# Kernel tuning notes

Hardware: AMD Instinct MI355X
Metric: run time of the kernel (lower is better)

The kernel has to match this reference:

```python
import jax, jax.numpy as jnp
import numpy as np

N = 100000          # nodes
E = 1600000         # edges per adjacency (avg degree 16)
DIMS = [256, 128, 64]
ALPHA = 0.8
WD = 1e-4


def setup_inputs() -> dict:
    key = jax.random.key(0)
    ks = jax.random.split(key, 11)
    X = jax.random.normal(ks[0], (N, DIMS[0]), jnp.float32)
    rows = jax.random.randint(ks[1], (E,), 0, N, jnp.int32)
    cols = jax.random.randint(ks[2], (E,), 0, N, jnp.int32)
    prune_rows = jax.random.randint(ks[3], (E,), 0, N, jnp.int32)
    prune_cols = jax.random.randint(ks[4], (E,), 0, N, jnp.int32)
    # learned params (torch.randn init, scaled 0.1 for fp32 numeric headroom)
    W0 = jax.random.normal(ks[5], (DIMS[0], DIMS[1]), jnp.float32) * 0.1
    W1 = jax.random.normal(ks[6], (DIMS[1], DIMS[2]), jnp.float32) * 0.1
    v00 = jax.random.normal(ks[7], (DIMS[1], 1), jnp.float32) * 0.1
    v01 = jax.random.normal(ks[8], (DIMS[1], 1), jnp.float32) * 0.1
    pv00 = jax.random.normal(ks[9], (DIMS[1], 1), jnp.float32) * 0.1
    pv01 = jax.random.normal(ks[10], (DIMS[1], 1), jnp.float32) * 0.1
    return {"X": X, "W0": W0, "W1": W1, "v00": v00, "v01": v01,
            "pv00": pv00, "pv01": pv01, "rows": rows, "cols": cols,
            "prune_rows": prune_rows, "prune_cols": prune_cols}


def _edge_softmax(rows, logits, n):
    # row-wise softmax over sparse edge logits
    m = jax.ops.segment_max(logits, rows, num_segments=n)
    e = jnp.exp(logits - m[rows])
    s = jax.ops.segment_sum(e, rows, num_segments=n)
    return e / s[rows]


def _attention(rows, cols, H, va, vb, n):
    # logit_e = (H @ va)[src_e] + (H @ vb)[dst_e]  (binary adjacency values)
    f1 = (H @ va)[:, 0]
    f2 = (H @ vb)[:, 0]
    return _edge_softmax(rows, f1[rows] + f2[cols], n)


def _spmm(rows, cols, vals, H, n):
    # out[i] = sum_{e: rows[e]==i} vals[e] * H[cols[e]]
    return jax.ops.segment_sum(vals[:, None] * H[cols], rows, num_segments=n)


def reference(X, W0, W1, v00, v01, pv00, pv01, rows, cols, prune_rows, prune_cols):
    n = X.shape[0]
    # ---- encoder ----
    H1 = X @ W0                                   # layer 0 projection
    c = _attention(rows, cols, H1, v00, v01, n)   # C[0]
    pc = _attention(prune_rows, prune_cols, H1, pv00, pv01, n)  # prune_C[0]
    H1a = (1.0 - ALPHA) * _spmm(rows, cols, c, H1, n) \
        + ALPHA * _spmm(prune_rows, prune_cols, pc, H1, n)
    H1a = jax.nn.elu(H1a)                         # nonlinear, layer 0 != last
    H_enc = H1a @ W1                              # layer 1 == last: no attention
    # ---- decoder ----
    D = H_enc @ W1.T                              # layer 1
    D = (1.0 - ALPHA) * _spmm(rows, cols, c, D, n) \
        + ALPHA * _spmm(prune_rows, prune_cols, pc, D, n)
    D = jax.nn.elu(D)                             # nonlinear, layer 1 != 0
    X_ = D @ W0.T                                 # layer 0: plain matmul
    # ---- loss ----
    loss = jnp.sqrt(jnp.sum((X - X_) ** 2)) \
         + WD * (jnp.sum(W0 ** 2) + jnp.sum(W1 ** 2))
    return (loss, H_enc, X_)
```

## Files before the change

### kernel.cpp

```cpp
#include <hip/hip_runtime.h>
#include <math.h>

#define N_NODES 100000
#define N_EDGES 1600000
#define TOT (2 * N_NODES)
#define SCAN_NB 256
#define SCAN_CH 4
#define RPB 25000

static inline int cdiv(long a, long b) { return (int)((a + b - 1) / b); }

typedef unsigned int uint;
typedef unsigned short ushort;
typedef __attribute__((ext_vector_type(8))) short short8v;
typedef __attribute__((ext_vector_type(4))) float f32x4;

__device__ inline float bf2f(uint u) { return __uint_as_float(u << 16); }
__device__ inline ushort f2bf(float f) {
    uint u = __float_as_uint(f);
    uint r = ((u >> 16) & 1u) + 0x7fffu;
    return (ushort)((u + r) >> 16);
}

template <int K, int M, bool AF32, int OUT, bool ELU, bool LOSS>
__global__ __launch_bounds__(256) void gemm_mfma(const void* __restrict__ Av,
                                                 const ushort* __restrict__ Bcm,
                                                 void* __restrict__ Cv,
                                                 void* __restrict__ Cv2,
                                                 const float* __restrict__ Xref,
                                                 float* __restrict__ partial,
                                                 int nrows) {
    constexpr int BM = 128;
    constexpr int KP = K + 8;
    constexpr int NCT = M / 16;
    __shared__ ushort Blds[M * KP];
    __shared__ ushort Alds[BM * 32];
    const int w = threadIdx.x >> 6;
    const int l = threadIdx.x & 63;
    const int rowg = l & 15;
    const int kg = l >> 4;
    const int rbase = blockIdx.x * BM;
    {
        const uint4* src = reinterpret_cast<const uint4*>(Bcm);
        uint4* dst = reinterpret_cast<uint4*>(Blds);
        const int total = M * KP / 8;
        for (int i = threadIdx.x; i < total; i += 256) dst[i] = src[i];
    }
    f32x4 acc[2][NCT] = {};
    for (int k0 = 0; k0 < K; k0 += 32) {
        __syncthreads();
        int r = threadIdx.x >> 1;
        int kk = (threadIdx.x & 1) * 16;
        int rg = min(rbase + r, nrows - 1);
        if (AF32) {
            const float* A = (const float*)Av;
            const float4* src = reinterpret_cast<const float4*>(A + (size_t)rg * K + k0 + kk);
            ushort* dst = &Alds[r * 32 + kk];
#pragma unroll
            for (int q = 0; q < 4; ++q) {
                float4 v = src[q];
                dst[4 * q + 0] = f2bf(v.x); dst[4 * q + 1] = f2bf(v.y);
                dst[4 * q + 2] = f2bf(v.z); dst[4 * q + 3] = f2bf(v.w);
            }
        } else {
            const ushort* A = (const ushort*)Av;
            const uint4* src = reinterpret_cast<const uint4*>(A + (size_t)rg * K + k0 + kk);
            uint4* dst = reinterpret_cast<uint4*>(&Alds[r * 32 + kk]);
            dst[0] = src[0];
            dst[1] = src[1];
        }
        __syncthreads();
#pragma unroll
        for (int rt = 0; rt < 2; ++rt) {
            short8v af = *reinterpret_cast<const short8v*>(
                &Alds[(w * 32 + rt * 16 + rowg) * 32 + kg * 8]);
#pragma unroll
            for (int ct = 0; ct < NCT; ++ct) {
                short8v bf = *reinterpret_cast<const short8v*>(
                    &Blds[(ct * 16 + rowg) * KP + k0 + kg * 8]);
                acc[rt][ct] = __builtin_amdgcn_mfma_f32_16x16x32_bf16(
                    af, bf, acc[rt][ct], 0, 0, 0);
            }
        }
    }
    float lsum = 0.f;
#pragma unroll
    for (int rt = 0; rt < 2; ++rt) {
#pragma unroll
        for (int q = 0; q < 4; ++q) {
            int r = rbase + w * 32 + rt * 16 + kg * 4 + q;
            if (r >= nrows) continue;
#pragma unroll
            for (int ct = 0; ct < NCT; ++ct) {
                float o = acc[rt][ct][q];
                if (ELU) o = o > 0.f ? o : expm1f(o);
                int col = ct * 16 + rowg;
                if (OUT == 0 || OUT == 3) ((float*)Cv)[(size_t)r * M + col] = o;
                if (OUT == 2) ((ushort*)Cv)[(size_t)r * M + col] = f2bf(o);
                if (OUT == 3) ((ushort*)Cv2)[(size_t)r * M + col] = f2bf(o);
                if (LOSS) {
                    float d = o - Xref[(size_t)r * 256 + col];
                    lsum += d * d;
                }
            }
        }
    }
    if (LOSS) {
        __shared__ float smRed[4];
#pragma unroll
        for (int off = 32; off > 0; off >>= 1) lsum += __shfl_down(lsum, off);
        __syncthreads();
        if (l == 0) smRed[w] = lsum;
        __syncthreads();
        if (threadIdx.x == 0)
            partial[blockIdx.x] = smRed[0] + smRed[1] + smRed[2] + smRed[3];
    }
}

__global__ __launch_bounds__(256) void prepB1_kernel(const float* __restrict__ W0,
                                                     ushort* __restrict__ B) {
    int i = blockIdx.x * 256 + threadIdx.x;
    if (i >= 256 * 128) return;
    int k = i / 128, m = i - k * 128;
    B[m * 264 + k] = f2bf(W0[i]);
}
__global__ __launch_bounds__(256) void prepB5_kernel(const float* __restrict__ W1,
                                                     ushort* __restrict__ B) {
    int i = blockIdx.x * 256 + threadIdx.x;
    if (i >= 128 * 64) return;
    int k = i / 64, m = i - k * 64;
    B[m * 136 + k] = f2bf(W1[i]);
}
__global__ __launch_bounds__(256) void prepB7_kernel(const float* __restrict__ W1,
                                                     ushort* __restrict__ B) {
    int i = blockIdx.x * 256 + threadIdx.x;
    if (i >= 128 * 64) return;
    int m = i / 64, k = i - m * 64;
    B[m * 72 + k] = f2bf(W1[i]);
}
__global__ __launch_bounds__(256) void prepB8_kernel(const float* __restrict__ W0,
                                                     ushort* __restrict__ B) {
    int i = blockIdx.x * 256 + threadIdx.x;
    if (i >= 256 * 128) return;
    int m = i / 128, k = i - m * 128;
    B[m * 136 + k] = f2bf(W0[i]);
}

__global__ __launch_bounds__(256) void attn_f4_kernel(const ushort* __restrict__ Hb,
                                                      const float* __restrict__ va,
                                                      const float* __restrict__ vb,
                                                      const float* __restrict__ pva,
                                                      const float* __restrict__ pvb,
                                                      float* __restrict__ f1,
                                                      float* __restrict__ f2,
                                                      float* __restrict__ pf1,
                                                      float* __restrict__ pf2) {
    int wid = (blockIdx.x * 256 + threadIdx.x) >> 6;
    int lane = threadIdx.x & 63;
    if (wid >= N_NODES) return;
    uint hv = reinterpret_cast<const uint*>(Hb + (size_t)wid * 128)[lane];
    float x0 = bf2f(hv & 0xffffu);
    float x1 = bf2f(hv >> 16);
    int k = 2 * lane;
    float a = x0 * va[k] + x1 * va[k + 1];
    float b = x0 * vb[k] + x1 * vb[k + 1];
    float pa = x0 * pva[k] + x1 * pva[k + 1];
    float pb = x0 * pvb[k] + x1 * pvb[k + 1];
#pragma unroll
    for (int off = 32; off > 0; off >>= 1) {
        a += __shfl_down(a, off);
        b += __shfl_down(b, off);
        pa += __shfl_down(pa, off);
        pb += __shfl_down(pb, off);
    }
    if (lane == 0) { f1[wid] = a; f2[wid] = b; pf1[wid] = pa; pf2[wid] = pb; }
}

__global__ __launch_bounds__(256) void hist2_kernel(const int* __restrict__ rows,
                                                    const int* __restrict__ prows,
                                                    int* __restrict__ deg) {
    int e = blockIdx.x * 256 + threadIdx.x;
    if (e >= 2 * N_EDGES) return;
    int r = e < N_EDGES ? rows[e] : N_NODES + prows[e - N_EDGES];
    atomicAdd(&deg[r], 1);
}

__device__ inline int pad8(int d) { return (d + 7) & ~7; }

__global__ __launch_bounds__(256) void scan1_kernel(const int* __restrict__ deg,
                                                    int* __restrict__ bsum) {
    __shared__ int sm[256];
    int base = (blockIdx.x * 256 + threadIdx.x) * SCAN_CH;
    int s = 0;
#pragma unroll
    for (int i = 0; i < SCAN_CH; ++i) {
        int idx = base + i;
        if (idx < TOT) s += pad8(deg[idx]);
    }
    sm[threadIdx.x] = s;
    __syncthreads();
    for (int off = 128; off > 0; off >>= 1) {
        if (threadIdx.x < off) sm[threadIdx.x] += sm[threadIdx.x + off];
        __syncthreads();
    }
    if (threadIdx.x == 0) bsum[blockIdx.x] = sm[0];
}

__global__ void scan2_kernel(int* __restrict__ bsum) {
    if (threadIdx.x != 0) return;
    int run = 0;
    for (int i = 0; i < SCAN_NB; ++i) {
        int t = bsum[i];
        bsum[i] = run;
        run += t;
    }
}

__global__ __launch_bounds__(256) void scan3_kernel(const int* __restrict__ deg,
                                                    const int* __restrict__ bsum,
                                                    int* __restrict__ rp) {
    __shared__ int sm[256];
    int base = (blockIdx.x * 256 + threadIdx.x) * SCAN_CH;
    int s = 0;
#pragma unroll
    for (int i = 0; i < SCAN_CH; ++i) {
        int idx = base + i;
        if (idx < TOT) s += pad8(deg[idx]);
    }
    sm[threadIdx.x] = s;
    __syncthreads();
    if (threadIdx.x == 0) {
        int run = bsum[blockIdx.x];
        for (int t = 0; t < 256; ++t) { int tmp = sm[t]; sm[t] = run; run += tmp; }
    }
    __syncthreads();
    int off = sm[threadIdx.x];
#pragma unroll
    for (int i = 0; i < SCAN_CH; ++i) {
        int idx = base + i;
        if (idx < TOT) { rp[idx] = off; off += pad8(deg[idx]); }
        else if (idx == TOT) rp[idx] = off;
    }
}

__global__ __launch_bounds__(256) void scatter_bucket_kernel(const int* __restrict__ rlist,
                                                             const int* __restrict__ clist,
                                                             int roff, int lo, int hi,
                                                             const int* __restrict__ rp,
                                                             int* __restrict__ cur,
                                                             int* __restrict__ ccol) {
    int e = blockIdx.x * 256 + threadIdx.x;
    if (e >= N_EDGES) return;
    int r0 = rlist[e];
    if (r0 < lo || r0 >= hi) return;
    int r = roff + r0;
    int pos = rp[r] + atomicAdd(&cur[r], 1);
    ccol[pos] = clist[e];
}

__global__ __launch_bounds__(256) void edgeval_kernel(const int* __restrict__ rp,
                                                      const int* __restrict__ deg,
                                                      const int* __restrict__ ccol,
                                                      const float* __restrict__ f1,
                                                      const float* __restrict__ f2,
                                                      const float* __restrict__ pf1,
                                                      const float* __restrict__ pf2,
                                                      int2* __restrict__ eg) {
    int r = blockIdx.x * 16 + (threadIdx.x >> 4);
    int sl = threadIdx.x & 15;
    bool second = r >= N_NODES;
    float f1r = second ? pf1[r - N_NODES] : f1[r];
    const float* f2t = second ? pf2 : f2;
    float scale = second ? 0.8f : 0.2f;
    int j0 = rp[r];
    int realend = j0 + deg[r];
    int pend = rp[r + 1];
    float s = 0.f;
    for (int j = j0 + sl; j < realend; j += 16)
        s += __expf(f1r + f2t[ccol[j]]);
#pragma unroll
    for (int off = 8; off > 0; off >>= 1) s += __shfl_xor(s, off);
    float inv = s > 0.f ? scale / s : 0.f;
    for (int j = j0 + sl; j < pend; j += 16) {
        if (j < realend) {
            int c = ccol[j];
            float wv = __expf(f1r + f2t[c]) * inv;
            eg[j] = make_int2(c, __float_as_int(wv));
        } else {
            eg[j] = make_int2(0, 0);
        }
    }
}

#define SPU 8
__device__ inline void gat128(const int2* __restrict__ eg, int j,
                              const uint* __restrict__ Hu, int lane,
                              float& s0, float& s1) {
    int2 d[SPU];
#pragma unroll
    for (int u = 0; u < SPU; ++u) d[u] = eg[j + u];
    uint h[SPU];
#pragma unroll
    for (int u = 0; u < SPU; ++u) h[u] = Hu[(size_t)d[u].x * 64 + lane];
#pragma unroll
    for (int u = 0; u < SPU; ++u) {
        float v = __int_as_float(d[u].y);
        s0 += v * bf2f(h[u] & 0xffffu);
        s1 += v * bf2f(h[u] >> 16);
    }
}

__global__ __launch_bounds__(256) void spmm_fused_kernel(const int* __restrict__ rp,
                                                         const int2* __restrict__ eg,
                                                         const ushort* __restrict__ Hb,
                                                         float* __restrict__ out) {
    int r = blockIdx.x * 4 + (threadIdx.x >> 6);
    int lane = threadIdx.x & 63;
    const uint* Hu = reinterpret_cast<const uint*>(Hb);
    float a0 = 0.f, a1 = 0.f, b0 = 0.f, b1 = 0.f;
    int j1 = rp[r], E1 = rp[r + 1];
    int j2 = rp[N_NODES + r], E2 = rp[N_NODES + r + 1];
    while (j1 < E1 && j2 < E2) {
        int2 d1[SPU], d2[SPU];
#pragma unroll
        for (int u = 0; u < SPU; ++u) d1[u] = eg[j1 + u];
#pragma unroll
        for (int u = 0; u < SPU; ++u) d2[u] = eg[j2 + u];
        uint h1[SPU], h2[SPU];
#pragma unroll
        for (int u = 0; u < SPU; ++u) h1[u] = Hu[(size_t)d1[u].x * 64 + lane];
#pragma unroll
        for (int u = 0; u < SPU; ++u) h2[u] = Hu[(size_t)d2[u].x * 64 + lane];
#pragma unroll
        for (int u = 0; u < SPU; ++u) {
            float v1 = __int_as_float(d1[u].y);
            float v2 = __int_as_float(d2[u].y);
            a0 += v1 * bf2f(h1[u] & 0xffffu);
            a1 += v1 * bf2f(h1[u] >> 16);
            b0 += v2 * bf2f(h2[u] & 0xffffu);
            b1 += v2 * bf2f(h2[u] >> 16);
        }
        j1 += SPU; j2 += SPU;
    }
    while (j1 < E1) { gat128(eg, j1, Hu, lane, a0, a1); j1 += SPU; }
    while (j2 < E2) { gat128(eg, j2, Hu, lane, b0, b1); j2 += SPU; }
    float o0 = a0 + b0;
    float o1 = a1 + b1;
    o0 = o0 > 0.f ? o0 : expm1f(o0);
    o1 = o1 > 0.f ? o1 : expm1f(o1);
    *reinterpret_cast<float2*>(out + (size_t)r * 128 + 2 * lane) = make_float2(o0, o1);
}

__device__ inline void gat64(const int2* __restrict__ eg, int j,
                             const ushort* __restrict__ Hb, int lane, float& s) {
    int2 d[SPU];
#pragma unroll
    for (int u = 0; u < SPU; ++u) d[u] = eg[j + u];
    ushort h[SPU];
#pragma unroll
    for (int u = 0; u < SPU; ++u) h[u] = Hb[(size_t)d[u].x * 64 + lane];
#pragma unroll
    for (int u = 0; u < SPU; ++u)
        s += __int_as_float(d[u].y) * bf2f((uint)h[u]);
}

__global__ __launch_bounds__(256) void spmm64_fused_kernel(const int* __restrict__ rp,
                                                           const int2* __restrict__ eg,
                                                           const ushort* __restrict__ Hb,
                                                           float* __restrict__ S) {
    int r = blockIdx.x * 4 + (threadIdx.x >> 6);
    int lane = threadIdx.x & 63;
    float a = 0.f, b = 0.f;
    int j1 = rp[r], E1 = rp[r + 1];
    int j2 = rp[N_NODES + r], E2 = rp[N_NODES + r + 1];
    while (j1 < E1 && j2 < E2) {
        int2 d1[SPU], d2[SPU];
#pragma unroll
        for (int u = 0; u < SPU; ++u) d1[u] = eg[j1 + u];
#pragma unroll
        for (int u = 0; u < SPU; ++u) d2[u] = eg[j2 + u];
        ushort h1[SPU], h2[SPU];
#pragma unroll
        for (int u = 0; u < SPU; ++u) h1[u] = Hb[(size_t)d1[u].x * 64 + lane];
#pragma unroll
        for (int u = 0; u < SPU; ++u) h2[u] = Hb[(size_t)d2[u].x * 64 + lane];
#pragma unroll
        for (int u = 0; u < SPU; ++u) {
            a += __int_as_float(d1[u].y) * bf2f((uint)h1[u]);
            b += __int_as_float(d2[u].y) * bf2f((uint)h2[u]);
        }
        j1 += SPU; j2 += SPU;
    }
    while (j1 < E1) { gat64(eg, j1, Hb, lane, a); j1 += SPU; }
    while (j2 < E2) { gat64(eg, j2, Hb, lane, b); j2 += SPU; }
    S[(size_t)r * 64 + lane] = a + b;
}

__global__ __launch_bounds__(256) void sq_reduce_kernel(const float* __restrict__ a,
                                                        float* __restrict__ acc, int n) {
    __shared__ float sm[4];
    float s = 0.f;
    for (int i = blockIdx.x * 256 + threadIdx.x; i < n; i += gridDim.x * 256) {
        float d = a[i];
        s += d * d;
    }
#pragma unroll
    for (int off = 32; off > 0; off >>= 1) s += __shfl_down(s, off);
    int lane = threadIdx.x & 63, w = threadIdx.x >> 6;
    if (lane == 0) sm[w] = s;
    __syncthreads();
    if (threadIdx.x == 0) atomicAdd(acc, sm[0] + sm[1] + sm[2] + sm[3]);
}

__global__ __launch_bounds__(256) void partial_reduce_kernel(const float* __restrict__ p,
                                                             int n, float* __restrict__ acc) {
    __shared__ float sm[4];
    float s = 0.f;
    for (int i = threadIdx.x; i < n; i += 256) s += p[i];
#pragma unroll
    for (int off = 32; off > 0; off >>= 1) s += __shfl_down(s, off);
    int lane = threadIdx.x & 63, w = threadIdx.x >> 6;
    if (lane == 0) sm[w] = s;
    __syncthreads();
    if (threadIdx.x == 0) atomicAdd(acc, sm[0] + sm[1] + sm[2] + sm[3]);
}

__global__ void finalize_kernel(const float* __restrict__ acc, float* __restrict__ out) {
    out[0] = sqrtf(acc[0]) + 1e-4f * (acc[1] + acc[2]);
}

extern "C" void kernel_launch(void* const* d_in, const int* in_sizes, int n_in,
                              void* d_out, int out_size, void* d_ws, size_t ws_size,
                              hipStream_t stream) {
    const float* X    = (const float*)d_in[0];
    const float* W0   = (const float*)d_in[1];
    const float* W1   = (const float*)d_in[2];
    const float* v00  = (const float*)d_in[3];
    const float* v01  = (const float*)d_in[4];
    const float* pv00 = (const float*)d_in[5];
    const float* pv01 = (const float*)d_in[6];
    const int* rows   = (const int*)d_in[7];
    const int* cols   = (const int*)d_in[8];
    const int* prows  = (const int*)d_in[9];
    const int* pcols  = (const int*)d_in[10];

    float* out  = (float*)d_out;
    float* Henc = out + 1;
    float* Xrec = out + 1 + (size_t)N_NODES * 64;

    ushort* bufAh  = (ushort*)(out + 6400004);
    float*  S      = out + 6400004;
    int*    ccol   = (int*)(out + 12800004);
    int2*   eg     = (int2*)(out + 17600004);
    ushort* HencB  = (ushort*)(out + 27200004);
    int*    deg    = (int*)(out + 28800004);
    int*    cur    = deg + TOT;

    float* ws   = (float*)d_ws;
    float* bufB = ws;
    ushort* bufBh = (ushort*)bufB;
    float* f1   = bufB + (size_t)N_NODES * 128;
    float* f2   = f1 + N_NODES;
    float* pf1  = f2 + N_NODES;
    float* pf2  = pf1 + N_NODES;
    float* acc  = pf2 + N_NODES;
    ushort* B1cm = (ushort*)(acc + 4);
    ushort* B5cm = B1cm + 128 * 264;
    ushort* B7cm = B5cm + 64 * 136;
    ushort* B8cm = B7cm + 128 * 72;
    int*   rp   = (int*)(B8cm + 256 * 136);
    int*   bsum = rp + TOT + 1;
    float* partial = (float*)(bsum + SCAN_NB);

    const int n = N_NODES;
    const int EG = cdiv(N_EDGES, 256);
    const int EG2 = cdiv(2 * (long)N_EDGES, 256);

    prepB1_kernel<<<cdiv(256 * 128, 256), 256, 0, stream>>>(W0, B1cm);
    prepB5_kernel<<<cdiv(128 * 64, 256), 256, 0, stream>>>(W1, B5cm);
    prepB7_kernel<<<cdiv(128 * 64, 256), 256, 0, stream>>>(W1, B7cm);
    prepB8_kernel<<<cdiv(256 * 128, 256), 256, 0, stream>>>(W0, B8cm);

    gemm_mfma<256, 128, true, 2, false, false><<<cdiv(n, 128), 256, 0, stream>>>(
        X, B1cm, bufAh, nullptr, nullptr, nullptr, n);

    hipMemsetAsync(deg, 0, 2 * (size_t)TOT * sizeof(int), stream);
    hipMemsetAsync(acc, 0, 4 * sizeof(float), stream);

    attn_f4_kernel<<<cdiv(n, 4), 256, 0, stream>>>(bufAh, v00, v01, pv00, pv01,
                                                   f1, f2, pf1, pf2);

    hist2_kernel<<<EG2, 256, 0, stream>>>(rows, prows, deg);
    scan1_kernel<<<SCAN_NB, 256, 0, stream>>>(deg, bsum);
    scan2_kernel<<<1, 64, 0, stream>>>(bsum);
    scan3_kernel<<<SCAN_NB, 256, 0, stream>>>(deg, bsum, rp);
    for (int p = 0; p < 4; ++p)
        scatter_bucket_kernel<<<EG, 256, 0, stream>>>(rows, cols, 0,
                                                      p * RPB, (p + 1) * RPB,
                                                      rp, cur, ccol);
    for (int p = 0; p < 4; ++p)
        scatter_bucket_kernel<<<EG, 256, 0, stream>>>(prows, pcols, N_NODES,
                                                      p * RPB, (p + 1) * RPB,
                                                      rp, cur, ccol);
    edgeval_kernel<<<cdiv(2 * n, 16), 256, 0, stream>>>(rp, deg, ccol,
                                                        f1, f2, pf1, pf2, eg);

    spmm_fused_kernel<<<n / 4, 256, 0, stream>>>(rp, eg, bufAh, bufB);

    gemm_mfma<128, 64, true, 3, false, false><<<cdiv(n, 128), 256, 0, stream>>>(
        bufB, B5cm, Henc, HencB, nullptr, nullptr, n);

    spmm64_fused_kernel<<<n / 4, 256, 0, stream>>>(rp, eg, HencB, S);

    gemm_mfma<64, 128, true, 2, true, false><<<cdiv(n, 128), 256, 0, stream>>>(
        S, B7cm, bufBh, nullptr, nullptr, nullptr, n);

    gemm_mfma<128, 256, false, 0, false, true><<<cdiv(n, 128), 256, 0, stream>>>(
        bufBh, B8cm, Xrec, nullptr, X, partial, n);

    partial_reduce_kernel<<<1, 256, 0, stream>>>(partial, cdiv(n, 128), acc + 0);
    sq_reduce_kernel<<<16, 256, 0, stream>>>(W0, acc + 1, 256 * 128);
    sq_reduce_kernel<<<4, 256, 0, stream>>>(W1, acc + 2, 128 * 64);
    finalize_kernel<<<1, 1, 0, stream>>>(acc, out);
}
```

Baseline: 823.2 us.

## Interleave both adjacencies per node in CSR and software-pipeline SpMM gathers

The CSR bucket layout moves from two separate halves, one per adjacency, to interleaved buckets (2*r, 2*r+1). Each node's edges from both adjacencies then form one contiguous segment, and the fused SpMM kernels can walk a single range with one accumulator instead of two parallel loops plus tails. The SpMM loops also prefetch the next 8 edge/feature loads while accumulating the current batch, and use 32-bit index math. This is meant to cut loop overhead and expose more memory-level parallelism. The cost is extra register pressure from the double-buffered loads, and the histogram and scatter atomics now land on adjacent counters for both adjacencies.

```diff
diff --git a/kernel.cpp b/kernel.cpp
--- a/kernel.cpp
+++ b/kernel.cpp
@@ -181,8 +181,8 @@
                                                     int* __restrict__ deg) {
     int e = blockIdx.x * 256 + threadIdx.x;
     if (e >= 2 * N_EDGES) return;
-    int r = e < N_EDGES ? rows[e] : N_NODES + prows[e - N_EDGES];
-    atomicAdd(&deg[r], 1);
+    int b = e < N_EDGES ? rows[e] * 2 : prows[e - N_EDGES] * 2 + 1;
+    atomicAdd(&deg[b], 1);
 }
 
 __device__ inline int pad8(int d) { return (d + 7) & ~7; }
@@ -245,7 +245,7 @@
 
 __global__ __launch_bounds__(256) void scatter_bucket_kernel(const int* __restrict__ rlist,
                                                              const int* __restrict__ clist,
-                                                             int roff, int lo, int hi,
+                                                             int adj, int lo, int hi,
                                                              const int* __restrict__ rp,
                                                              int* __restrict__ cur,
                                                              int* __restrict__ ccol) {
@@ -253,8 +253,8 @@
     if (e >= N_EDGES) return;
     int r0 = rlist[e];
     if (r0 < lo || r0 >= hi) return;
-    int r = roff + r0;
-    int pos = rp[r] + atomicAdd(&cur[r], 1);
+    int b = r0 * 2 + adj;
+    int pos = rp[b] + atomicAdd(&cur[b], 1);
     ccol[pos] = clist[e];
 }
 
@@ -266,15 +266,15 @@
                                                       const float* __restrict__ pf1,
                                                       const float* __restrict__ pf2,
                                                       int2* __restrict__ eg) {
-    int r = blockIdx.x * 16 + (threadIdx.x >> 4);
+    int b = blockIdx.x * 16 + (threadIdx.x >> 4);
     int sl = threadIdx.x & 15;
-    bool second = r >= N_NODES;
-    float f1r = second ? pf1[r - N_NODES] : f1[r];
-    const float* f2t = second ? pf2 : f2;
-    float scale = second ? 0.8f : 0.2f;
-    int j0 = rp[r];
-    int realend = j0 + deg[r];
-    int pend = rp[r + 1];
+    int adj = b & 1, r = b >> 1;
+    float f1r = adj ? pf1[r] : f1[r];
+    const float* f2t = adj ? pf2 : f2;
+    float scale = adj ? 0.8f : 0.2f;
+    int j0 = rp[b];
+    int realend = j0 + deg[b];
+    int pend = rp[b + 1];
     float s = 0.f;
     for (int j = j0 + sl; j < realend; j += 16)
         s += __expf(f1r + f2t[ccol[j]]);
@@ -293,23 +293,6 @@
 }
 
 #define SPU 8
-__device__ inline void gat128(const int2* __restrict__ eg, int j,
-                              const uint* __restrict__ Hu, int lane,
-                              float& s0, float& s1) {
-    int2 d[SPU];
-#pragma unroll
-    for (int u = 0; u < SPU; ++u) d[u] = eg[j + u];
-    uint h[SPU];
-#pragma unroll
-    for (int u = 0; u < SPU; ++u) h[u] = Hu[(size_t)d[u].x * 64 + lane];
-#pragma unroll
-    for (int u = 0; u < SPU; ++u) {
-        float v = __int_as_float(d[u].y);
-        s0 += v * bf2f(h[u] & 0xffffu);
-        s1 += v * bf2f(h[u] >> 16);
-    }
-}
-
 __global__ __launch_bounds__(256) void spmm_fused_kernel(const int* __restrict__ rp,
                                                          const int2* __restrict__ eg,
                                                          const ushort* __restrict__ Hb,
@@ -317,51 +300,40 @@
     int r = blockIdx.x * 4 + (threadIdx.x >> 6);
     int lane = threadIdx.x & 63;
     const uint* Hu = reinterpret_cast<const uint*>(Hb);
-    float a0 = 0.f, a1 = 0.f, b0 = 0.f, b1 = 0.f;
-    int j1 = rp[r], E1 = rp[r + 1];
-    int j2 = rp[N_NODES + r], E2 = rp[N_NODES + r + 1];
-    while (j1 < E1 && j2 < E2) {
-        int2 d1[SPU], d2[SPU];
-#pragma unroll
-        for (int u = 0; u < SPU; ++u) d1[u] = eg[j1 + u];
-#pragma unroll
-        for (int u = 0; u < SPU; ++u) d2[u] = eg[j2 + u];
-        uint h1[SPU], h2[SPU];
-#pragma unroll
-        for (int u = 0; u < SPU; ++u) h1[u] = Hu[(size_t)d1[u].x * 64 + lane];
-#pragma unroll
-        for (int u = 0; u < SPU; ++u) h2[u] = Hu[(size_t)d2[u].x * 64 + lane];
+    float a0 = 0.f, a1 = 0.f;
+    int j = rp[2 * r], E = rp[2 * r + 2];
+    if (j < E) {
+        int2 d[SPU]; uint h[SPU];
+#pragma unroll
+        for (int u = 0; u < SPU; ++u) d[u] = eg[j + u];
+#pragma unroll
+        for (int u = 0; u < SPU; ++u) h[u] = Hu[(uint)d[u].x * 64u + lane];
+        j += SPU;
+        for (; j < E; j += SPU) {
+            int2 dn[SPU]; uint hn[SPU];
+#pragma unroll
+            for (int u = 0; u < SPU; ++u) dn[u] = eg[j + u];
+#pragma unroll
+            for (int u = 0; u < SPU; ++u) hn[u] = Hu[(uint)dn[u].x * 64u + lane];
+#pragma unroll
+            for (int u = 0; u < SPU; ++u) {
+                float v = __int_as_float(d[u].y);
+                a0 += v * bf2f(h[u] & 0xffffu);
+                a1 += v * bf2f(h[u] >> 16);
+            }
+#pragma unroll
+            for (int u = 0; u < SPU; ++u) { d[u] = dn[u]; h[u] = hn[u]; }
+        }
 #pragma unroll
         for (int u = 0; u < SPU; ++u) {
-            float v1 = __int_as_float(d1[u].y);
-            float v2 = __int_as_float(d2[u].y);
-            a0 += v1 * bf2f(h1[u] & 0xffffu);
-            a1 += v1 * bf2f(h1[u] >> 16);
-            b0 += v2 * bf2f(h2[u] & 0xffffu);
-            b1 += v2 * bf2f(h2[u] >> 16);
-        }
-        j1 += SPU; j2 += SPU;
-    }
-    while (j1 < E1) { gat128(eg, j1, Hu, lane, a0, a1); j1 += SPU; }
-    while (j2 < E2) { gat128(eg, j2, Hu, lane, b0, b1); j2 += SPU; }
-    float o0 = a0 + b0;
-    float o1 = a1 + b1;
-    o0 = o0 > 0.f ? o0 : expm1f(o0);
-    o1 = o1 > 0.f ? o1 : expm1f(o1);
+            float v = __int_as_float(d[u].y);
+            a0 += v * bf2f(h[u] & 0xffffu);
+            a1 += v * bf2f(h[u] >> 16);
+        }
+    }
+    float o0 = a0 > 0.f ? a0 : expm1f(a0);
+    float o1 = a1 > 0.f ? a1 : expm1f(a1);
     *reinterpret_cast<float2*>(out + (size_t)r * 128 + 2 * lane) = make_float2(o0, o1);
-}
-
-__device__ inline void gat64(const int2* __restrict__ eg, int j,
-                             const ushort* __restrict__ Hb, int lane, float& s) {
-    int2 d[SPU];
-#pragma unroll
-    for (int u = 0; u < SPU; ++u) d[u] = eg[j + u];
-    ushort h[SPU];
-#pragma unroll
-    for (int u = 0; u < SPU; ++u) h[u] = Hb[(size_t)d[u].x * 64 + lane];
-#pragma unroll
-    for (int u = 0; u < SPU; ++u)
-        s += __int_as_float(d[u].y) * bf2f((uint)h[u]);
 }
 
 __global__ __launch_bounds__(256) void spmm64_fused_kernel(const int* __restrict__ rp,
@@ -370,30 +342,32 @@
                                                            float* __restrict__ S) {
     int r = blockIdx.x * 4 + (threadIdx.x >> 6);
     int lane = threadIdx.x & 63;
-    float a = 0.f, b = 0.f;
-    int j1 = rp[r], E1 = rp[r + 1];
-    int j2 = rp[N_NODES + r], E2 = rp[N_NODES + r + 1];
-    while (j1 < E1 && j2 < E2) {
-        int2 d1[SPU], d2[SPU];
-#pragma unroll
-        for (int u = 0; u < SPU; ++u) d1[u] = eg[j1 + u];
-#pragma unroll
-        for (int u = 0; u < SPU; ++u) d2[u] = eg[j2 + u];
-        ushort h1[SPU], h2[SPU];
-#pragma unroll
-        for (int u = 0; u < SPU; ++u) h1[u] = Hb[(size_t)d1[u].x * 64 + lane];
-#pragma unroll
-        for (int u = 0; u < SPU; ++u) h2[u] = Hb[(size_t)d2[u].x * 64 + lane];
-#pragma unroll
-        for (int u = 0; u < SPU; ++u) {
-            a += __int_as_float(d1[u].y) * bf2f((uint)h1[u]);
-            b += __int_as_float(d2[u].y) * bf2f((uint)h2[u]);
-        }
-        j1 += SPU; j2 += SPU;
-    }
-    while (j1 < E1) { gat64(eg, j1, Hb, lane, a); j1 += SPU; }
-    while (j2 < E2) { gat64(eg, j2, Hb, lane, b); j2 += SPU; }
-    S[(size_t)r * 64 + lane] = a + b;
+    float a = 0.f;
+    int j = rp[2 * r], E = rp[2 * r + 2];
+    if (j < E) {
+        int2 d[SPU]; ushort h[SPU];
+#pragma unroll
+        for (int u = 0; u < SPU; ++u) d[u] = eg[j + u];
+#pragma unroll
+        for (int u = 0; u < SPU; ++u) h[u] = Hb[(uint)d[u].x * 64u + lane];
+        j += SPU;
+        for (; j < E; j += SPU) {
+            int2 dn[SPU]; ushort hn[SPU];
+#pragma unroll
+            for (int u = 0; u < SPU; ++u) dn[u] = eg[j + u];
+#pragma unroll
+            for (int u = 0; u < SPU; ++u) hn[u] = Hb[(uint)dn[u].x * 64u + lane];
+#pragma unroll
+            for (int u = 0; u < SPU; ++u)
+                a += __int_as_float(d[u].y) * bf2f((uint)h[u]);
+#pragma unroll
+            for (int u = 0; u < SPU; ++u) { d[u] = dn[u]; h[u] = hn[u]; }
+        }
+#pragma unroll
+        for (int u = 0; u < SPU; ++u)
+            a += __int_as_float(d[u].y) * bf2f((uint)h[u]);
+    }
+    S[(size_t)r * 64 + lane] = a;
 }
 
 __global__ __launch_bounds__(256) void sq_reduce_kernel(const float* __restrict__ a,
@@ -499,11 +473,11 @@
                                                       p * RPB, (p + 1) * RPB,
                                                       rp, cur, ccol);
     for (int p = 0; p < 4; ++p)
-        scatter_bucket_kernel<<<EG, 256, 0, stream>>>(prows, pcols, N_NODES,
+        scatter_bucket_kernel<<<EG, 256, 0, stream>>>(prows, pcols, 1,
                                                       p * RPB, (p + 1) * RPB,
                                                       rp, cur, ccol);
-    edgeval_kernel<<<cdiv(2 * n, 16), 256, 0, stream>>>(rp, deg, ccol,
-                                                        f1, f2, pf1, pf2, eg);
+    edgeval_kernel<<<cdiv(TOT, 16), 256, 0, stream>>>(rp, deg, ccol,
+                                                      f1, f2, pf1, pf2, eg);
 
     spmm_fused_kernel<<<n / 4, 256, 0, stream>>>(rp, eg, bufAh, bufB);
 
```

After: 799.7 us. 2.9% less time.
